# Optimization experiments

Measured on AMD Instinct MI355X. Metric: run time of the kernel, lower is better.

Reference implementation:

```python
import jax, jax.numpy as jnp
import numpy as np
import math

B, L, S, T = 16, 256, 128, 128
Q_DIM, F_DIM, H_DIM, OUT_DIM = 512, 512, 512, 512


def setup_inputs() -> dict:
    key = jax.random.key(0)
    ks = jax.random.split(key, 10)
    inp = {
        "query": jax.random.normal(ks[0], (B, L, Q_DIM), dtype=jnp.float32),
        "src": jax.random.normal(ks[1], (B, S, F_DIM), dtype=jnp.float32),
        "trg": jax.random.normal(ks[2], (B, T, F_DIM), dtype=jnp.float32),
        # LinearAct params (Linear + identity act; out layer uses tanh)
        "Wq": jax.random.normal(ks[3], (Q_DIM, H_DIM), dtype=jnp.float32) / math.sqrt(Q_DIM),
        "bq": jnp.zeros((H_DIM,), dtype=jnp.float32),
        "Ws": jax.random.normal(ks[4], (F_DIM, H_DIM), dtype=jnp.float32) / math.sqrt(F_DIM),
        "bs": jnp.zeros((H_DIM,), dtype=jnp.float32),
        "Wt": jax.random.normal(ks[5], (F_DIM, H_DIM), dtype=jnp.float32) / math.sqrt(F_DIM),
        "bt": jnp.zeros((H_DIM,), dtype=jnp.float32),
        "Wo": jax.random.normal(ks[6], (2 * H_DIM + Q_DIM, OUT_DIM), dtype=jnp.float32) / math.sqrt(2 * H_DIM + Q_DIM),
        "bo": jnp.zeros((OUT_DIM,), dtype=jnp.float32),
    }
    return inp


def reference(query, src, trg, Wq, bq, Ws, bs, Wt, bt, Wo, bo):
    b, l, _ = query.shape
    _, s, f = src.shape
    _, t, _ = trg.shape
    hid_dim = Wq.shape[1]

    q = query @ Wq + bq                              # b, l, h
    # pad one all-zero feature row onto src and trg (as in torch.cat with pad_tensor)
    pad = jnp.zeros((b, 1, f), dtype=src.dtype)
    src_p = jnp.concatenate([src, pad], axis=1)       # b, s+1, f
    trg_p = jnp.concatenate([trg, pad], axis=1)       # b, t+1, f
    s_key = src_p @ Ws + bs                           # b, s+1, h
    t_key = trg_p @ Wt + bt                           # b, t+1, h

    # trilinear scores: b, l, s+1, t+1
    weight = jnp.einsum('blk,bsk,btk->blst', q, s_key, t_key) / math.sqrt(hid_dim)
    # joint softmax over the flattened (s+1)*(t+1) axis
    weight = jax.nn.softmax(weight.reshape(b, l, -1), axis=-1).reshape(b, l, s + 1, t + 1)

    s_ctx = jnp.einsum('blst,bsk->blk', weight, s_key)  # b, l, h
    t_ctx = jnp.einsum('blst,btk->blk', weight, t_key)  # b, l, h

    x = jnp.concatenate([query, s_ctx, t_ctx], axis=-1)  # b, l, q+2h
    return jnp.tanh(x @ Wo + bo)
```

## Files before the change

kernel.cpp:

```cpp
#include <hip/hip_runtime.h>
#include <math.h>

#define HD 512
#define SP 129
#define RPAD 144
#define WPAD 160
#define NBATCH 16
#define MQ 4096
#define SCALE 0.04419417382415922f

typedef _Float16 f16;
typedef _Float16 f16x8 __attribute__((ext_vector_type(8)));
typedef _Float16 f16x4 __attribute__((ext_vector_type(4)));
typedef float f32x4  __attribute__((ext_vector_type(4)));

__device__ __forceinline__ void gload_lds16(const f16* g, f16* l) {
  __builtin_amdgcn_global_load_lds(
      (const __attribute__((address_space(1))) void*)g,
      (__attribute__((address_space(3))) void*)l, 16, 0, 0);
}

__global__ __launch_bounds__(256) void conv_f32_f16(
    const float* __restrict__ a, f16* __restrict__ o, int n)
{
  int base = (blockIdx.x * 256 + threadIdx.x) * 8;
  if (base < n) {
    float4 x = *(const float4*)(a + base);
    float4 y = *(const float4*)(a + base + 4);
    f16x8 v = { (f16)x.x, (f16)x.y, (f16)x.z, (f16)x.w,
                (f16)y.x, (f16)y.y, (f16)y.z, (f16)y.w };
    *(f16x8*)(o + base) = v;
  }
}

__global__ __launch_bounds__(256) void convT_f32_f16(
    const float* __restrict__ W, f16* __restrict__ WT, int K, int N)
{
  __shared__ float t[64][65];
  const int k0 = blockIdx.x * 64, n0 = blockIdx.y * 64;
  const int tid = threadIdx.x;
  const int r = tid >> 4, c4 = (tid & 15) * 4;
  #pragma unroll
  for (int i = 0; i < 4; ++i) {
    int k = r + 16*i;
    float4 v = *(const float4*)(W + (size_t)(k0 + k)*N + n0 + c4);
    t[k][c4] = v.x; t[k][c4+1] = v.y; t[k][c4+2] = v.z; t[k][c4+3] = v.w;
  }
  __syncthreads();
  #pragma unroll
  for (int i = 0; i < 4; ++i) {
    int n = r + 16*i;
    f16x4 v = { (f16)t[c4][n], (f16)t[c4+1][n], (f16)t[c4+2][n], (f16)t[c4+3][n] };
    *(f16x4*)(WT + (size_t)(n0 + n)*K + k0 + c4) = v;
  }
}

template<int NSEG, int MODE>
__global__ __launch_bounds__(256) void gemm_f16(
    const f16* __restrict__ A0, const f16* __restrict__ A1,
    const f16* __restrict__ A2, const f16* __restrict__ WT,
    const float* __restrict__ bias, void* __restrict__ Cv,
    f16* __restrict__ CT, int M, int N)
{
  __shared__ __align__(16) f16 As[64*64];
  __shared__ __align__(16) f16 Bs[64*64];
  const int KTOT = NSEG * 512;
  const int tid  = threadIdx.x;
  const int lane = tid & 63;
  const int w    = tid >> 6;
  const int wr   = w & 1, wc = w >> 1;
  const int fq   = lane >> 4, fr = lane & 15;
  const int bm = blockIdx.x * 64, bn = blockIdx.y * 64;

  f32x4 acc[2][2] = {};

  for (int k0 = 0; k0 < KTOT; k0 += 64) {
    const int seg  = k0 >> 9;
    const f16* Ap  = (NSEG == 1) ? A0 : (seg == 0 ? A0 : (seg == 1 ? A1 : A2));
    const int kloc = k0 & 511;
    #pragma unroll
    for (int i = 0; i < 2; ++i) {
      int idx = tid + 256*i;
      int r = idx >> 3, c = idx & 7;
      const uint4 va = *(const uint4*)(Ap + (size_t)(bm + r)*512 + kloc + c*8);
      const uint4 vb = *(const uint4*)(WT + (size_t)(bn + r)*KTOT + k0 + c*8);
      int o = ((r << 7) + (c << 4)) ^ ((r & 7) << 4);
      *(uint4*)((char*)As + o) = va;
      *(uint4*)((char*)Bs + o) = vb;
    }
    __syncthreads();
    #pragma unroll
    for (int ks = 0; ks < 2; ++ks) {
      f16x8 af[2], bf_[2];
      #pragma unroll
      for (int i = 0; i < 2; ++i) {
        int ra = wr*32 + i*16 + fr;
        int oa = ((ra << 7) + (ks << 6) + (fq << 4)) ^ ((ra & 7) << 4);
        af[i] = *(const f16x8*)((const char*)As + oa);
        int rb = wc*32 + i*16 + fr;
        int ob = ((rb << 7) + (ks << 6) + (fq << 4)) ^ ((rb & 7) << 4);
        bf_[i] = *(const f16x8*)((const char*)Bs + ob);
      }
      #pragma unroll
      for (int i = 0; i < 2; ++i)
        #pragma unroll
        for (int j = 0; j < 2; ++j)
          acc[i][j] = __builtin_amdgcn_mfma_f32_16x16x32_f16(af[i], bf_[j], acc[i][j], 0, 0, 0);
    }
    __syncthreads();
  }

  #pragma unroll
  for (int i = 0; i < 2; ++i) {
    #pragma unroll
    for (int j = 0; j < 2; ++j) {
      int n = bn + wc*32 + j*16 + fr;
      float bv = bias[n];
      if (MODE == 3) {
        const int m0 = bm + wr*32 + i*16 + fq*4;
        f16 vals[4];
        #pragma unroll
        for (int r = 0; r < 4; ++r) {
          int m = m0 + r;
          f16 x = (f16)(acc[i][j][r] + bv);
          vals[r] = x;
          int mo = (m >> 7) * RPAD + (m & 127);
          ((f16*)Cv)[(size_t)mo*N + n] = x;
        }
        f16x4 v4 = { vals[0], vals[1], vals[2], vals[3] };
        *(f16x4*)(CT + ((size_t)(m0 >> 7)*512 + n)*WPAD + (m0 & 127)) = v4;
      } else {
        #pragma unroll
        for (int r = 0; r < 4; ++r) {
          int m = bm + wr*32 + i*16 + fq*4 + r;
          float x = acc[i][j][r] + bv;
          if (MODE == 0) {
            ((f16*)Cv)[(size_t)m*N + n] = (f16)x;
          } else {
            x = fminf(fmaxf(x, -20.f), 20.f);
            float e = __expf(2.0f * x);
            ((float*)Cv)[(size_t)m*N + n] = (e - 1.0f) / (e + 1.0f);
          }
        }
      }
    }
  }
}

__global__ void write_pad_f16(f16* __restrict__ skey, const float* __restrict__ bs,
                              f16* __restrict__ tkey, const float* __restrict__ bt,
                              f16* __restrict__ skeyT, f16* __restrict__ tkeyT)
{
  int i = blockIdx.x * 256 + threadIdx.x;
  int b = i >> 9, n = i & 511;
  for (int r = 128; r < RPAD; ++r) {
    skey[((size_t)b*RPAD + r)*HD + n] = (r == 128) ? (f16)bs[n] : (f16)0.f;
    tkey[((size_t)b*RPAD + r)*HD + n] = (r == 128) ? (f16)bt[n] : (f16)0.f;
  }
  size_t o = ((size_t)b*512 + n)*WPAD;
  for (int c = 128; c < WPAD; ++c) {
    skeyT[o + c] = (c == 128) ? (f16)bs[n] : (f16)0.f;
    tkeyT[o + c] = (c == 128) ? (f16)bt[n] : (f16)0.f;
  }
}

__global__ __launch_bounds__(256) void border_kernel(
    const f16* __restrict__ q_h, const f16* __restrict__ skey,
    const f16* __restrict__ tkey, float* __restrict__ Sb)
{
  const int blk = blockIdx.x;
  const int b = blk >> 3, z = (blk >> 2) & 1, mt = blk & 3;
  const f16* keys = (z ? skey : tkey) + (size_t)b*RPAD*HD;
  const f16* u    = (z ? tkey : skey) + ((size_t)b*RPAD + 128)*HD;
  const int gid0 = b*256 + mt*64;

  __shared__ __align__(16) f16 Ks[RPAD*32];
  const int tid = threadIdx.x, lane = tid & 63, w = tid >> 6;
  const int fq = lane >> 4, fr = lane & 15;

  f32x4 acc[9] = {};

  for (int kt = 0; kt < 16; ++kt) {
    uint4 t0, t1, t2;
    {
      int r0 = tid >> 2, c0 = tid & 3;
      t0 = *(const uint4*)(keys + (size_t)r0*HD + kt*32 + c0*8);
      int r1 = (tid + 256) >> 2, c1 = tid & 3;
      t1 = *(const uint4*)(keys + (size_t)r1*HD + kt*32 + c1*8);
      if (tid < 64) {
        int r2 = (tid + 512) >> 2, c2 = tid & 3;
        t2 = *(const uint4*)(keys + (size_t)r2*HD + kt*32 + c2*8);
      }
    }
    __syncthreads();
    {
      int r0 = tid >> 2, c0 = tid & 3;
      *(uint4*)(&Ks[r0*32 + c0*8]) = t0;
      int r1 = (tid + 256) >> 2;
      *(uint4*)(&Ks[r1*32 + c0*8]) = t1;
      if (tid < 64) {
        int r2 = (tid + 512) >> 2;
        *(uint4*)(&Ks[r2*32 + c0*8]) = t2;
      }
    }
    __syncthreads();
    const f16x8 qf = *(const f16x8*)(q_h + (size_t)(gid0 + w*16 + fr)*HD + kt*32 + fq*8);
    const f16x8 uv = *(const f16x8*)(u + kt*32 + fq*8);
    const f16x8 a = qf * uv;
    #pragma unroll
    for (int j = 0; j < 9; ++j) {
      const f16x8 bfr = *(const f16x8*)(&Ks[(j*16 + fr)*32 + fq*8]);
      acc[j] = __builtin_amdgcn_mfma_f32_16x16x32_f16(a, bfr, acc[j], 0, 0, 0);
    }
  }

  float* dst = Sb + (size_t)z*MQ*RPAD;
  #pragma unroll
  for (int j = 0; j < 9; ++j)
    #pragma unroll
    for (int r = 0; r < 4; ++r)
      dst[(size_t)(gid0 + w*16 + fq*4 + r)*RPAD + j*16 + fr] = acc[j][r];
}

__global__ __launch_bounds__(256, 4) void attn_core(
    const f16* __restrict__ qg,
    const f16* __restrict__ skey,
    const f16* __restrict__ tkey,
    const float* __restrict__ Sb,
    f16* __restrict__ wsn,
    f16* __restrict__ wtn)
{
  __shared__ __align__(16) f16 KB[2*2*128*32];
  __shared__ __align__(16) f16 qs[HD];
  __shared__ float wsA[2][128];
  __shared__ float wtA[2][128];
  __shared__ float redA[4], redB[4], redC[4], redD[4], redE[4];
  __shared__ float cornerP;

  const int tid  = threadIdx.x;
  const int lane = tid & 63;
  const int w    = tid >> 6;
  const int rb   = w & 1;
  const int cb   = w >> 1;
  const int fq   = lane >> 4;
  const int fr   = lane & 15;

  const int gid = ((int)blockIdx.x & 7) * 512 + ((int)blockIdx.x >> 3);
  const int b   = gid >> 8;
  const f16* skg = skey + (size_t)b * RPAD * HD;
  const f16* tkg = tkey + (size_t)b * RPAD * HD;

  if (tid < 64) *(uint4*)(qs + tid*8) = *(const uint4*)(qg + (size_t)gid*HD + tid*8);

  auto stage = [&](int kt, int buf) {
    #pragma unroll
    for (int n = 0; n < 4; ++n) {
      int idx = w*4 + n;
      int key = idx >> 3;
      int rg  = idx & 7;
      const f16* g = (key ? tkg : skg)
                   + (size_t)(rg*16 + (lane >> 2))*HD + kt*32 + (lane & 3)*8;
      f16* l = &KB[((buf*2 + key)*128 + rg*16)*32];
      gload_lds16(g, l);
    }
  };

  f32x4 acc[4][4] = {};

  auto mfma_kt = [&](int kt, int cur) {
    const f16x8 qv = *(const f16x8*)(&qs[kt*32 + fq*8]);
    const int abase = (cur*2 + 0)*128*32;
    const int bbase = (cur*2 + 1)*128*32;
    f16x8 B[4];
    #pragma unroll
    for (int j = 0; j < 4; ++j) {
      int rt = cb*64 + j*16 + fr;
      B[j] = *(const f16x8*)(&KB[bbase + rt*32 + fq*8]);
    }
    __builtin_amdgcn_s_setprio(1);
    #pragma unroll
    for (int i = 0; i < 4; ++i) {
      int rs = rb*64 + i*16 + fr;
      const f16x8 raw = *(const f16x8*)(&KB[abase + rs*32 + fq*8]);
      const f16x8 a = raw * qv;
      #pragma unroll
      for (int j = 0; j < 4; ++j)
        acc[i][j] = __builtin_amdgcn_mfma_f32_16x16x32_f16(a, B[j], acc[i][j], 0, 0, 0);
    }
    __builtin_amdgcn_s_setprio(0);
  };

  stage(0, 0);
  __syncthreads();

  for (int kt = 0; kt < 16; ++kt) {
    const int cur = kt & 1;
    if (kt < 15) {
      stage(kt + 1, cur ^ 1);
      asm volatile("s_waitcnt vmcnt(4)" ::: "memory");
    } else {
      asm volatile("s_waitcnt vmcnt(0)" ::: "memory");
    }
    __builtin_amdgcn_s_barrier();
    mfma_kt(kt, cur);
    __builtin_amdgcn_s_barrier();
  }

  float m = -3e38f;
  #pragma unroll
  for (int i = 0; i < 4; ++i)
    #pragma unroll
    for (int j = 0; j < 4; ++j)
      #pragma unroll
      for (int r = 0; r < 4; ++r) m = fmaxf(m, acc[i][j][r]);
  #pragma unroll
  for (int off = 32; off > 0; off >>= 1) m = fmaxf(m, __shfl_xor(m, off));
  if (lane == 0) redA[w] = m;

  const float* SbT = Sb + (size_t)gid*RPAD;
  const float* SbS = Sb + (size_t)MQ*RPAD + (size_t)gid*RPAD;
  const float btv = (tid < 129) ? SbT[tid] : -3e38f;
  const float bsv = (tid < 128) ? SbS[tid] : -3e38f;
  float bm = fmaxf(btv, bsv);
  #pragma unroll
  for (int off = 32; off > 0; off >>= 1) bm = fmaxf(bm, __shfl_xor(bm, off));
  if (lane == 0) redB[w] = bm;
  __syncthreads();
  const float mraw = fmaxf(
      fmaxf(fmaxf(redA[0], redA[1]), fmaxf(redA[2], redA[3])),
      fmaxf(fmaxf(redB[0], redB[1]), fmaxf(redB[2], redB[3])));

  float csum = 0.f;
  #pragma unroll
  for (int i = 0; i < 4; ++i)
    #pragma unroll
    for (int j = 0; j < 4; ++j)
      #pragma unroll
      for (int r = 0; r < 4; ++r) {
        float p = __expf((acc[i][j][r] - mraw) * SCALE);
        acc[i][j][r] = p;
        csum += p;
      }
  #pragma unroll
  for (int off = 32; off > 0; off >>= 1) csum += __shfl_xor(csum, off);
  if (lane == 0) redC[w] = csum;

  #pragma unroll
  for (int i = 0; i < 4; ++i) {
    #pragma unroll
    for (int r = 0; r < 4; ++r) {
      float rs = acc[i][0][r] + acc[i][1][r] + acc[i][2][r] + acc[i][3][r];
      rs += __shfl_xor(rs, 1); rs += __shfl_xor(rs, 2);
      rs += __shfl_xor(rs, 4); rs += __shfl_xor(rs, 8);
      if (fr == 0) wsA[cb][rb*64 + i*16 + fq*4 + r] = rs;
    }
  }
  #pragma unroll
  for (int j = 0; j < 4; ++j) {
    float cs = 0.f;
    #pragma unroll
    for (int i = 0; i < 4; ++i)
      #pragma unroll
      for (int r = 0; r < 4; ++r) cs += acc[i][j][r];
    cs += __shfl_xor(cs, 16); cs += __shfl_xor(cs, 32);
    if (fq == 0) wtA[rb][cb*64 + j*16 + fr] = cs;
  }

  const float pbt = (tid < 129) ? __expf((btv - mraw) * SCALE) : 0.f;
  const float pbs = (tid < 128) ? __expf((bsv - mraw) * SCALE) : 0.f;
  float sbt = pbt, sbs = pbs;
  #pragma unroll
  for (int off = 32; off > 0; off >>= 1) {
    sbt += __shfl_xor(sbt, off);
    sbs += __shfl_xor(sbs, off);
  }
  if (lane == 0) { redD[w] = sbt; redE[w] = sbs; }
  if (tid == 128) cornerP = pbt;
  __syncthreads();

  const float pbt_sum = redD[0] + redD[1] + redD[2] + redD[3];
  const float pbs_sum = redE[0] + redE[1] + redE[2] + redE[3];
  const float core_sum = redC[0] + redC[1] + redC[2] + redC[3];
  const float invZ = 1.0f / (core_sum + pbt_sum + pbs_sum);

  if (tid < WPAD) {
    float wsv = (tid < 128) ? (wsA[0][tid] + wsA[1][tid] + pbs)
              : (tid == 128) ? pbt_sum : 0.f;
    float wtv = (tid < 128) ? (wtA[0][tid] + wtA[1][tid] + pbt)
              : (tid == 128) ? (pbs_sum + cornerP) : 0.f;
    wsn[(size_t)gid*WPAD + tid] = (f16)(wsv * invZ);
    wtn[(size_t)gid*WPAD + tid] = (f16)(wtv * invZ);
  }
}

__global__ __launch_bounds__(256) void ctx_gemm(
    const f16* __restrict__ wsn, const f16* __restrict__ wtn,
    const f16* __restrict__ skeyT, const f16* __restrict__ tkeyT,
    f16* __restrict__ sctx, f16* __restrict__ tctx)
{
  __shared__ __align__(16) f16 As[64*168];
  __shared__ __align__(16) f16 Bs[64*168];
  const int z = blockIdx.x & 1, b = blockIdx.x >> 1;
  const int mt = blockIdx.y, nt = blockIdx.z;
  const int tid = threadIdx.x, lane = tid & 63, w = tid >> 6;
  const int wr = w & 1, wc = w >> 1;
  const int fq = lane >> 4, fr = lane & 15;

  const f16* A  = (z ? wtn : wsn) + ((size_t)b*256 + mt*64)*WPAD;
  const f16* Bt = (z ? tkeyT : skeyT) + ((size_t)b*512 + nt*64)*WPAD;

  for (int t = tid; t < 1280; t += 256) {
    int r = t / 20, c = t % 20;
    *(uint4*)(&As[r*168 + c*8]) = *(const uint4*)(A + (size_t)r*WPAD + c*8);
    *(uint4*)(&Bs[r*168 + c*8]) = *(const uint4*)(Bt + (size_t)r*WPAD + c*8);
  }
  __syncthreads();

  f32x4 acc[2][2] = {};
  #pragma unroll
  for (int ks = 0; ks < 5; ++ks) {
    f16x8 af[2], bf_[2];
    #pragma unroll
    for (int i = 0; i < 2; ++i) {
      af[i]  = *(const f16x8*)(&As[(wr*32 + i*16 + fr)*168 + ks*32 + fq*8]);
      bf_[i] = *(const f16x8*)(&Bs[(wc*32 + i*16 + fr)*168 + ks*32 + fq*8]);
    }
    #pragma unroll
    for (int i = 0; i < 2; ++i)
      #pragma unroll
      for (int j = 0; j < 2; ++j)
        acc[i][j] = __builtin_amdgcn_mfma_f32_16x16x32_f16(af[i], bf_[j], acc[i][j], 0, 0, 0);
  }

  f16* out = z ? tctx : sctx;
  #pragma unroll
  for (int i = 0; i < 2; ++i)
    #pragma unroll
    for (int j = 0; j < 2; ++j) {
      int col = nt*64 + wc*32 + j*16 + fr;
      #pragma unroll
      for (int r = 0; r < 4; ++r) {
        int row = b*256 + mt*64 + wr*32 + i*16 + fq*4 + r;
        out[(size_t)row*HD + col] = (f16)acc[i][j][r];
      }
    }
}

extern "C" void kernel_launch(void* const* d_in, const int* in_sizes, int n_in,
                              void* d_out, int out_size, void* d_ws, size_t ws_size,
                              hipStream_t stream) {
  (void)in_sizes; (void)n_in; (void)out_size; (void)ws_size;
  const float* query = (const float*)d_in[0];
  const float* src   = (const float*)d_in[1];
  const float* trg   = (const float*)d_in[2];
  const float* Wq    = (const float*)d_in[3];
  const float* bq    = (const float*)d_in[4];
  const float* Wsm   = (const float*)d_in[5];
  const float* bs    = (const float*)d_in[6];
  const float* Wtm   = (const float*)d_in[7];
  const float* bt    = (const float*)d_in[8];
  const float* Wo    = (const float*)d_in[9];
  const float* bo    = (const float*)d_in[10];
  float* out = (float*)d_out;

  char* p = (char*)d_ws;
  f16* query_h = (f16*)p;                 p += (size_t)MQ*HD*2;
  f16* src_h   = (f16*)p;                 p += (size_t)2048*HD*2;
  f16* trg_h   = (f16*)p;                 p += (size_t)2048*HD*2;
  f16* WqT     = (f16*)p;                 p += (size_t)HD*HD*2;
  f16* WsT     = (f16*)p;                 p += (size_t)HD*HD*2;
  f16* WtT     = (f16*)p;                 p += (size_t)HD*HD*2;
  f16* WoT     = (f16*)p;                 p += (size_t)1536*HD*2;
  f16* q_h     = (f16*)p;                 p += (size_t)MQ*HD*2;
  f16* skey    = (f16*)p;                 p += (size_t)NBATCH*RPAD*HD*2;
  f16* tkey    = (f16*)p;                 p += (size_t)NBATCH*RPAD*HD*2;
  f16* skeyT   = (f16*)p;                 p += (size_t)NBATCH*HD*WPAD*2;
  f16* tkeyT   = (f16*)p;                 p += (size_t)NBATCH*HD*WPAD*2;
  f16* wsn     = (f16*)p;                 p += (size_t)MQ*WPAD*2;
  f16* wtn     = (f16*)p;                 p += (size_t)MQ*WPAD*2;
  f16* sctx    = (f16*)p;                 p += (size_t)MQ*HD*2;
  f16* tctx    = (f16*)p;                 p += (size_t)MQ*HD*2;
  float* Sb    = (float*)src_h;

  dim3 blk(256);
  conv_f32_f16<<<dim3(MQ*HD/8/256), blk, 0, stream>>>(query, query_h, MQ*HD);
  conv_f32_f16<<<dim3(2048*HD/8/256), blk, 0, stream>>>(src, src_h, 2048*HD);
  conv_f32_f16<<<dim3(2048*HD/8/256), blk, 0, stream>>>(trg, trg_h, 2048*HD);
  convT_f32_f16<<<dim3(8, 8), blk, 0, stream>>>(Wq, WqT, HD, HD);
  convT_f32_f16<<<dim3(8, 8), blk, 0, stream>>>(Wsm, WsT, HD, HD);
  convT_f32_f16<<<dim3(8, 8), blk, 0, stream>>>(Wtm, WtT, HD, HD);
  convT_f32_f16<<<dim3(24, 8), blk, 0, stream>>>(Wo, WoT, 1536, HD);

  gemm_f16<1,0><<<dim3(64, 8), blk, 0, stream>>>(query_h, nullptr, nullptr, WqT, bq, q_h, nullptr, MQ, HD);
  gemm_f16<1,3><<<dim3(32, 8), blk, 0, stream>>>(src_h, nullptr, nullptr, WsT, bs, skey, skeyT, 2048, HD);
  gemm_f16<1,3><<<dim3(32, 8), blk, 0, stream>>>(trg_h, nullptr, nullptr, WtT, bt, tkey, tkeyT, 2048, HD);
  write_pad_f16<<<dim3(32), blk, 0, stream>>>(skey, bs, tkey, bt, skeyT, tkeyT);

  border_kernel<<<dim3(128), blk, 0, stream>>>(q_h, skey, tkey, Sb);
  attn_core<<<dim3(MQ), blk, 0, stream>>>(q_h, skey, tkey, Sb, wsn, wtn);
  ctx_gemm<<<dim3(32, 4, 8), blk, 0, stream>>>(wsn, wtn, skeyT, tkeyT, sctx, tctx);

  gemm_f16<3,2><<<dim3(64, 8), blk, 0, stream>>>(query_h, sctx, tctx, WoT, bo, out, nullptr, MQ, HD);
}
```

Baseline: 199.7 us.

## Fuse f32→f16 conversion into GEMMs, merge prep launches, swizzle LDS, use exp2

Removes the separate activation-conversion kernels by converting fp32 query/src/trg to f16 inside the GEMM tile loads. Weight transposes and pad writes are merged into one prep kernel, and the three input projections into one launch, which cuts launch count. LDS layouts in border_kernel and attn_core get XOR swizzles to reduce bank conflicts, and exp is replaced by exp2f with prescaled constants. The trade-off is that fp32 activations are now read directly in the GEMMs, and query is re-read and re-converted in the output GEMM.

```diff
diff --git a/kernel.cpp b/kernel.cpp
--- a/kernel.cpp
+++ b/kernel.cpp
@@ -8,6 +8,8 @@
 #define NBATCH 16
 #define MQ 4096
 #define SCALE 0.04419417382415922f
+#define SCLG2E 0.06375871645788f
+#define TANH2E 2.8853900817779268f
 
 typedef _Float16 f16;
 typedef _Float16 f16x8 __attribute__((ext_vector_type(8)));
@@ -20,30 +22,44 @@
       (__attribute__((address_space(3))) void*)l, 16, 0, 0);
 }
 
-__global__ __launch_bounds__(256) void conv_f32_f16(
-    const float* __restrict__ a, f16* __restrict__ o, int n)
+__global__ __launch_bounds__(256) void prep_kernel(
+    const float* __restrict__ Wq, const float* __restrict__ Ws,
+    const float* __restrict__ Wt, const float* __restrict__ Wo,
+    const float* __restrict__ bs, const float* __restrict__ bt,
+    f16* __restrict__ WqT, f16* __restrict__ WsT,
+    f16* __restrict__ WtT, f16* __restrict__ WoT,
+    f16* __restrict__ skey, f16* __restrict__ tkey,
+    f16* __restrict__ skeyT, f16* __restrict__ tkeyT)
 {
-  int base = (blockIdx.x * 256 + threadIdx.x) * 8;
-  if (base < n) {
-    float4 x = *(const float4*)(a + base);
-    float4 y = *(const float4*)(a + base + 4);
-    f16x8 v = { (f16)x.x, (f16)x.y, (f16)x.z, (f16)x.w,
-                (f16)y.x, (f16)y.y, (f16)y.z, (f16)y.w };
-    *(f16x8*)(o + base) = v;
-  }
-}
-
-__global__ __launch_bounds__(256) void convT_f32_f16(
-    const float* __restrict__ W, f16* __restrict__ WT, int K, int N)
-{
+  const int id = blockIdx.x;
+  const int tid = threadIdx.x;
+  if (id >= 384) {
+    int i = (id - 384) * 256 + tid;
+    int b = i >> 9, n = i & 511;
+    for (int r = 128; r < RPAD; ++r) {
+      skey[((size_t)b*RPAD + r)*HD + n] = (r == 128) ? (f16)bs[n] : (f16)0.f;
+      tkey[((size_t)b*RPAD + r)*HD + n] = (r == 128) ? (f16)bt[n] : (f16)0.f;
+    }
+    size_t o = ((size_t)b*512 + n)*WPAD;
+    for (int c = 128; c < WPAD; ++c) {
+      skeyT[o + c] = (c == 128) ? (f16)bs[n] : (f16)0.f;
+      tkeyT[o + c] = (c == 128) ? (f16)bt[n] : (f16)0.f;
+    }
+    return;
+  }
+  const float* W; f16* WT; int K; int rest;
+  if (id < 64)       { W = Wq; WT = WqT; K = 512;  rest = id; }
+  else if (id < 128) { W = Ws; WT = WsT; K = 512;  rest = id - 64; }
+  else if (id < 192) { W = Wt; WT = WtT; K = 512;  rest = id - 128; }
+  else               { W = Wo; WT = WoT; K = 1536; rest = id - 192; }
+  const int k0 = (rest >> 3) * 64, n0 = (rest & 7) * 64;
+
   __shared__ float t[64][65];
-  const int k0 = blockIdx.x * 64, n0 = blockIdx.y * 64;
-  const int tid = threadIdx.x;
   const int r = tid >> 4, c4 = (tid & 15) * 4;
   #pragma unroll
   for (int i = 0; i < 4; ++i) {
     int k = r + 16*i;
-    float4 v = *(const float4*)(W + (size_t)(k0 + k)*N + n0 + c4);
+    float4 v = *(const float4*)(W + (size_t)(k0 + k)*512 + n0 + c4);
     t[k][c4] = v.x; t[k][c4+1] = v.y; t[k][c4+2] = v.z; t[k][c4+3] = v.w;
   }
   __syncthreads();
@@ -55,37 +71,46 @@
   }
 }
 
-template<int NSEG, int MODE>
-__global__ __launch_bounds__(256) void gemm_f16(
-    const f16* __restrict__ A0, const f16* __restrict__ A1,
-    const f16* __restrict__ A2, const f16* __restrict__ WT,
-    const float* __restrict__ bias, void* __restrict__ Cv,
-    f16* __restrict__ CT, int M, int N)
+__global__ __launch_bounds__(256) void gemm_in(
+    const float* __restrict__ query, const float* __restrict__ src,
+    const float* __restrict__ trg,
+    const f16* __restrict__ WqT, const f16* __restrict__ WsT,
+    const f16* __restrict__ WtT,
+    const float* __restrict__ bq, const float* __restrict__ bsv,
+    const float* __restrict__ btv,
+    f16* __restrict__ q_h, f16* __restrict__ skey, f16* __restrict__ tkey,
+    f16* __restrict__ skeyT, f16* __restrict__ tkeyT)
 {
   __shared__ __align__(16) f16 As[64*64];
   __shared__ __align__(16) f16 Bs[64*64];
-  const int KTOT = NSEG * 512;
+  const int x = blockIdx.x;
+  const float* A; const f16* WT; const float* bias; int bm; int iskey;
+  f16 *Ch, *CT;
+  if (x < 64)      { A = query; WT = WqT; bias = bq;  bm = x*64;      iskey = 0; Ch = q_h;  CT = nullptr; }
+  else if (x < 96) { A = src;   WT = WsT; bias = bsv; bm = (x-64)*64; iskey = 1; Ch = skey; CT = skeyT; }
+  else             { A = trg;   WT = WtT; bias = btv; bm = (x-96)*64; iskey = 1; Ch = tkey; CT = tkeyT; }
+  const int bn = blockIdx.y * 64;
   const int tid  = threadIdx.x;
   const int lane = tid & 63;
   const int w    = tid >> 6;
   const int wr   = w & 1, wc = w >> 1;
   const int fq   = lane >> 4, fr = lane & 15;
-  const int bm = blockIdx.x * 64, bn = blockIdx.y * 64;
 
   f32x4 acc[2][2] = {};
 
-  for (int k0 = 0; k0 < KTOT; k0 += 64) {
-    const int seg  = k0 >> 9;
-    const f16* Ap  = (NSEG == 1) ? A0 : (seg == 0 ? A0 : (seg == 1 ? A1 : A2));
-    const int kloc = k0 & 511;
+  for (int k0 = 0; k0 < 512; k0 += 64) {
     #pragma unroll
     for (int i = 0; i < 2; ++i) {
       int idx = tid + 256*i;
       int r = idx >> 3, c = idx & 7;
-      const uint4 va = *(const uint4*)(Ap + (size_t)(bm + r)*512 + kloc + c*8);
-      const uint4 vb = *(const uint4*)(WT + (size_t)(bn + r)*KTOT + k0 + c*8);
+      const float* ap = A + (size_t)(bm + r)*512 + k0 + c*8;
+      float4 x0 = *(const float4*)ap;
+      float4 x1 = *(const float4*)(ap + 4);
+      f16x8 va = { (f16)x0.x, (f16)x0.y, (f16)x0.z, (f16)x0.w,
+                   (f16)x1.x, (f16)x1.y, (f16)x1.z, (f16)x1.w };
+      const uint4 vb = *(const uint4*)(WT + (size_t)(bn + r)*512 + k0 + c*8);
       int o = ((r << 7) + (c << 4)) ^ ((r & 7) << 4);
-      *(uint4*)((char*)As + o) = va;
+      *(f16x8*)((char*)As + o) = va;
       *(uint4*)((char*)Bs + o) = vb;
     }
     __syncthreads();
@@ -116,16 +141,16 @@
     for (int j = 0; j < 2; ++j) {
       int n = bn + wc*32 + j*16 + fr;
       float bv = bias[n];
-      if (MODE == 3) {
+      if (iskey) {
         const int m0 = bm + wr*32 + i*16 + fq*4;
         f16 vals[4];
         #pragma unroll
         for (int r = 0; r < 4; ++r) {
           int m = m0 + r;
-          f16 x = (f16)(acc[i][j][r] + bv);
-          vals[r] = x;
+          f16 xx = (f16)(acc[i][j][r] + bv);
+          vals[r] = xx;
           int mo = (m >> 7) * RPAD + (m & 127);
-          ((f16*)Cv)[(size_t)mo*N + n] = x;
+          Ch[(size_t)mo*512 + n] = xx;
         }
         f16x4 v4 = { vals[0], vals[1], vals[2], vals[3] };
         *(f16x4*)(CT + ((size_t)(m0 >> 7)*512 + n)*WPAD + (m0 & 127)) = v4;
@@ -133,34 +158,10 @@
         #pragma unroll
         for (int r = 0; r < 4; ++r) {
           int m = bm + wr*32 + i*16 + fq*4 + r;
-          float x = acc[i][j][r] + bv;
-          if (MODE == 0) {
-            ((f16*)Cv)[(size_t)m*N + n] = (f16)x;
-          } else {
-            x = fminf(fmaxf(x, -20.f), 20.f);
-            float e = __expf(2.0f * x);
-            ((float*)Cv)[(size_t)m*N + n] = (e - 1.0f) / (e + 1.0f);
-          }
+          Ch[(size_t)m*512 + n] = (f16)(acc[i][j][r] + bv);
         }
       }
     }
-  }
-}
-
-__global__ void write_pad_f16(f16* __restrict__ skey, const float* __restrict__ bs,
-                              f16* __restrict__ tkey, const float* __restrict__ bt,
-                              f16* __restrict__ skeyT, f16* __restrict__ tkeyT)
-{
-  int i = blockIdx.x * 256 + threadIdx.x;
-  int b = i >> 9, n = i & 511;
-  for (int r = 128; r < RPAD; ++r) {
-    skey[((size_t)b*RPAD + r)*HD + n] = (r == 128) ? (f16)bs[n] : (f16)0.f;
-    tkey[((size_t)b*RPAD + r)*HD + n] = (r == 128) ? (f16)bt[n] : (f16)0.f;
-  }
-  size_t o = ((size_t)b*512 + n)*WPAD;
-  for (int c = 128; c < WPAD; ++c) {
-    skeyT[o + c] = (c == 128) ? (f16)bs[n] : (f16)0.f;
-    tkeyT[o + c] = (c == 128) ? (f16)bt[n] : (f16)0.f;
   }
 }
 
@@ -177,6 +178,8 @@
   __shared__ __align__(16) f16 Ks[RPAD*32];
   const int tid = threadIdx.x, lane = tid & 63, w = tid >> 6;
   const int fq = lane >> 4, fr = lane & 15;
+  const int wslot = ((tid & 3) ^ ((tid >> 3) & 3)) * 8;
+  const int rslot = ((fq ^ ((fr >> 1) & 3))) * 8;
 
   f32x4 acc[9] = {};
 
@@ -185,22 +188,22 @@
     {
       int r0 = tid >> 2, c0 = tid & 3;
       t0 = *(const uint4*)(keys + (size_t)r0*HD + kt*32 + c0*8);
-      int r1 = (tid + 256) >> 2, c1 = tid & 3;
-      t1 = *(const uint4*)(keys + (size_t)r1*HD + kt*32 + c1*8);
+      int r1 = (tid + 256) >> 2;
+      t1 = *(const uint4*)(keys + (size_t)r1*HD + kt*32 + c0*8);
       if (tid < 64) {
-        int r2 = (tid + 512) >> 2, c2 = tid & 3;
-        t2 = *(const uint4*)(keys + (size_t)r2*HD + kt*32 + c2*8);
+        int r2 = (tid + 512) >> 2;
+        t2 = *(const uint4*)(keys + (size_t)r2*HD + kt*32 + c0*8);
       }
     }
     __syncthreads();
     {
-      int r0 = tid >> 2, c0 = tid & 3;
-      *(uint4*)(&Ks[r0*32 + c0*8]) = t0;
+      int r0 = tid >> 2;
+      *(uint4*)(&Ks[r0*32 + wslot]) = t0;
       int r1 = (tid + 256) >> 2;
-      *(uint4*)(&Ks[r1*32 + c0*8]) = t1;
+      *(uint4*)(&Ks[r1*32 + wslot]) = t1;
       if (tid < 64) {
         int r2 = (tid + 512) >> 2;
-        *(uint4*)(&Ks[r2*32 + c0*8]) = t2;
+        *(uint4*)(&Ks[r2*32 + wslot]) = t2;
       }
     }
     __syncthreads();
@@ -209,7 +212,7 @@
     const f16x8 a = qf * uv;
     #pragma unroll
     for (int j = 0; j < 9; ++j) {
-      const f16x8 bfr = *(const f16x8*)(&Ks[(j*16 + fr)*32 + fq*8]);
+      const f16x8 bfr = *(const f16x8*)(&Ks[(j*16 + fr)*32 + rslot]);
       acc[j] = __builtin_amdgcn_mfma_f32_16x16x32_f16(a, bfr, acc[j], 0, 0, 0);
     }
   }
@@ -244,6 +247,8 @@
   const int cb   = w >> 1;
   const int fq   = lane >> 4;
   const int fr   = lane & 15;
+  const int so   = (fq ^ ((fr >> 1) & 3)) << 3;
+  const int gc   = ((lane & 3) ^ ((lane >> 3) & 3)) * 8;
 
   const int gid = ((int)blockIdx.x & 7) * 512 + ((int)blockIdx.x >> 3);
   const int b   = gid >> 8;
@@ -259,7 +264,7 @@
       int key = idx >> 3;
       int rg  = idx & 7;
       const f16* g = (key ? tkg : skg)
-                   + (size_t)(rg*16 + (lane >> 2))*HD + kt*32 + (lane & 3)*8;
+                   + (size_t)(rg*16 + (lane >> 2))*HD + kt*32 + gc;
       f16* l = &KB[((buf*2 + key)*128 + rg*16)*32];
       gload_lds16(g, l);
     }
@@ -275,13 +280,13 @@
     #pragma unroll
     for (int j = 0; j < 4; ++j) {
       int rt = cb*64 + j*16 + fr;
-      B[j] = *(const f16x8*)(&KB[bbase + rt*32 + fq*8]);
+      B[j] = *(const f16x8*)(&KB[bbase + rt*32 + so]);
     }
     __builtin_amdgcn_s_setprio(1);
     #pragma unroll
     for (int i = 0; i < 4; ++i) {
       int rs = rb*64 + i*16 + fr;
-      const f16x8 raw = *(const f16x8*)(&KB[abase + rs*32 + fq*8]);
+      const f16x8 raw = *(const f16x8*)(&KB[abase + rs*32 + so]);
       const f16x8 a = raw * qv;
       #pragma unroll
       for (int j = 0; j < 4; ++j)
@@ -337,7 +342,7 @@
     for (int j = 0; j < 4; ++j)
       #pragma unroll
       for (int r = 0; r < 4; ++r) {
-        float p = __expf((acc[i][j][r] - mraw) * SCALE);
+        float p = exp2f((acc[i][j][r] - mraw) * SCLG2E);
         acc[i][j][r] = p;
         csum += p;
       }
@@ -366,8 +371,8 @@
     if (fq == 0) wtA[rb][cb*64 + j*16 + fr] = cs;
   }
 
-  const float pbt = (tid < 129) ? __expf((btv - mraw) * SCALE) : 0.f;
-  const float pbs = (tid < 128) ? __expf((bsv - mraw) * SCALE) : 0.f;
+  const float pbt = (tid < 129) ? exp2f((btv - mraw) * SCLG2E) : 0.f;
+  const float pbs = (tid < 128) ? exp2f((bsv - mraw) * SCLG2E) : 0.f;
   float sbt = pbt, sbs = pbs;
   #pragma unroll
   for (int off = 32; off > 0; off >>= 1) {
@@ -442,6 +447,82 @@
       for (int r = 0; r < 4; ++r) {
         int row = b*256 + mt*64 + wr*32 + i*16 + fq*4 + r;
         out[(size_t)row*HD + col] = (f16)acc[i][j][r];
+      }
+    }
+}
+
+__global__ __launch_bounds__(256) void gemm_out(
+    const float* __restrict__ query, const f16* __restrict__ sctx,
+    const f16* __restrict__ tctx, const f16* __restrict__ WoT,
+    const float* __restrict__ bias, float* __restrict__ C)
+{
+  __shared__ __align__(16) f16 As[64*64];
+  __shared__ __align__(16) f16 Bs[64*64];
+  const int tid  = threadIdx.x;
+  const int lane = tid & 63;
+  const int w    = tid >> 6;
+  const int wr   = w & 1, wc = w >> 1;
+  const int fq   = lane >> 4, fr = lane & 15;
+  const int bm = blockIdx.x * 64, bn = blockIdx.y * 64;
+
+  f32x4 acc[2][2] = {};
+
+  for (int k0 = 0; k0 < 1536; k0 += 64) {
+    const int seg  = k0 >> 9;
+    const int kloc = k0 & 511;
+    #pragma unroll
+    for (int i = 0; i < 2; ++i) {
+      int idx = tid + 256*i;
+      int r = idx >> 3, c = idx & 7;
+      int o = ((r << 7) + (c << 4)) ^ ((r & 7) << 4);
+      if (seg == 0) {
+        const float* ap = query + (size_t)(bm + r)*512 + kloc + c*8;
+        float4 x0 = *(const float4*)ap;
+        float4 x1 = *(const float4*)(ap + 4);
+        f16x8 va = { (f16)x0.x, (f16)x0.y, (f16)x0.z, (f16)x0.w,
+                     (f16)x1.x, (f16)x1.y, (f16)x1.z, (f16)x1.w };
+        *(f16x8*)((char*)As + o) = va;
+      } else {
+        const f16* Ap = (seg == 1) ? sctx : tctx;
+        *(uint4*)((char*)As + o) = *(const uint4*)(Ap + (size_t)(bm + r)*512 + kloc + c*8);
+      }
+      *(uint4*)((char*)Bs + o) = *(const uint4*)(WoT + (size_t)(bn + r)*1536 + k0 + c*8);
+    }
+    __syncthreads();
+    #pragma unroll
+    for (int ks = 0; ks < 2; ++ks) {
+      f16x8 af[2], bf_[2];
+      #pragma unroll
+      for (int i = 0; i < 2; ++i) {
+        int ra = wr*32 + i*16 + fr;
+        int oa = ((ra << 7) + (ks << 6) + (fq << 4)) ^ ((ra & 7) << 4);
+        af[i] = *(const f16x8*)((const char*)As + oa);
+        int rb = wc*32 + i*16 + fr;
+        int ob = ((rb << 7) + (ks << 6) + (fq << 4)) ^ ((rb & 7) << 4);
+        bf_[i] = *(const f16x8*)((const char*)Bs + ob);
+      }
+      #pragma unroll
+      for (int i = 0; i < 2; ++i)
+        #pragma unroll
+        for (int j = 0; j < 2; ++j)
+          acc[i][j] = __builtin_amdgcn_mfma_f32_16x16x32_f16(af[i], bf_[j], acc[i][j], 0, 0, 0);
+    }
+    __syncthreads();
+  }
+
+  #pragma unroll
+  for (int i = 0; i < 2; ++i)
+    #pragma unroll
+    for (int j = 0; j < 2; ++j) {
+      int n = bn + wc*32 + j*16 + fr;
+      float bv = bias[n];
+      #pragma unroll
+      for (int r = 0; r < 4; ++r) {
+        int m = bm + wr*32 + i*16 + fq*4 + r;
+        float xx = acc[i][j][r] + bv;
+        xx = fminf(fmaxf(xx, -20.f), 20.f);
+        float e = exp2f(TANH2E * xx);
+        C[(size_t)m*HD + n] = (e - 1.0f) / (e + 1.0f);
       }
     }
 }
@@ -464,41 +545,30 @@
   float* out = (float*)d_out;
 
   char* p = (char*)d_ws;
-  f16* query_h = (f16*)p;                 p += (size_t)MQ*HD*2;
-  f16* src_h   = (f16*)p;                 p += (size_t)2048*HD*2;
-  f16* trg_h   = (f16*)p;                 p += (size_t)2048*HD*2;
-  f16* WqT     = (f16*)p;                 p += (size_t)HD*HD*2;
-  f16* WsT     = (f16*)p;                 p += (size_t)HD*HD*2;
-  f16* WtT     = (f16*)p;                 p += (size_t)HD*HD*2;
-  f16* WoT     = (f16*)p;                 p += (size_t)1536*HD*2;
-  f16* q_h     = (f16*)p;                 p += (size_t)MQ*HD*2;
-  f16* skey    = (f16*)p;                 p += (size_t)NBATCH*RPAD*HD*2;
-  f16* tkey    = (f16*)p;                 p += (size_t)NBATCH*RPAD*HD*2;
-  f16* skeyT   = (f16*)p;                 p += (size_t)NBATCH*HD*WPAD*2;
-  f16* tkeyT   = (f16*)p;                 p += (size_t)NBATCH*HD*WPAD*2;
-  f16* wsn     = (f16*)p;                 p += (size_t)MQ*WPAD*2;
-  f16* wtn     = (f16*)p;                 p += (size_t)MQ*WPAD*2;
-  f16* sctx    = (f16*)p;                 p += (size_t)MQ*HD*2;
-  f16* tctx    = (f16*)p;                 p += (size_t)MQ*HD*2;
-  float* Sb    = (float*)src_h;
+  f16* WqT   = (f16*)p;  p += (size_t)HD*HD*2;
+  f16* WsT   = (f16*)p;  p += (size_t)HD*HD*2;
+  f16* WtT   = (f16*)p;  p += (size_t)HD*HD*2;
+  f16* WoT   = (f16*)p;  p += (size_t)1536*HD*2;
+  f16* q_h   = (f16*)p;  p += (size_t)MQ*HD*2;
+  f16* skey  = (f16*)p;  p += (size_t)NBATCH*RPAD*HD*2;
+  f16* tkey  = (f16*)p;  p += (size_t)NBATCH*RPAD*HD*2;
+  f16* skeyT = (f16*)p;  p += (size_t)NBATCH*HD*WPAD*2;
+  f16* tkeyT = (f16*)p;  p += (size_t)NBATCH*HD*WPAD*2;
+  f16* wsn   = (f16*)p;  p += (size_t)MQ*WPAD*2;
+  f16* wtn   = (f16*)p;  p += (size_t)MQ*WPAD*2;
+  f16* sctx  = (f16*)p;  p += (size_t)MQ*HD*2;
+  f16* tctx  = (f16*)p;  p += (size_t)MQ*HD*2;
+  float* Sb  = (float*)p; p += (size_t)2*MQ*RPAD*4;
 
   dim3 blk(256);
-  conv_f32_f16<<<dim3(MQ*HD/8/256), blk, 0, stream>>>(query, query_h, MQ*HD);
-  conv_f32_f16<<<dim3(2048*HD/8/256), blk, 0, stream>>>(src, src_h, 2048*HD);
-  conv_f32_f16<<<dim3(2048*HD/8/256), blk, 0, stream>>>(trg, trg_h, 2048*HD);
-  convT_f32_f16<<<dim3(8, 8), blk, 0, stream>>>(Wq, WqT, HD, HD);
-  convT_f32_f16<<<dim3(8, 8), blk, 0, stream>>>(Wsm, WsT, HD, HD);
-  convT_f32_f16<<<dim3(8, 8), blk, 0, stream>>>(Wtm, WtT, HD, HD);
-  convT_f32_f16<<<dim3(24, 8), blk, 0, stream>>>(Wo, WoT, 1536, HD);
-
-  gemm_f16<1,0><<<dim3(64, 8), blk, 0, stream>>>(query_h, nullptr, nullptr, WqT, bq, q_h, nullptr, MQ, HD);
-  gemm_f16<1,3><<<dim3(32, 8), blk, 0, stream>>>(src_h, nullptr, nullptr, WsT, bs, skey, skeyT, 2048, HD);
-  gemm_f16<1,3><<<dim3(32, 8), blk, 0, stream>>>(trg_h, nullptr, nullptr, WtT, bt, tkey, tkeyT, 2048, HD);
-  write_pad_f16<<<dim3(32), blk, 0, stream>>>(skey, bs, tkey, bt, skeyT, tkeyT);
-
+  prep_kernel<<<dim3(416), blk, 0, stream>>>(Wq, Wsm, Wtm, Wo, bs, bt,
+                                             WqT, WsT, WtT, WoT,
+                                             skey, tkey, skeyT, tkeyT);
+  gemm_in<<<dim3(128, 8), blk, 0, stream>>>(query, src, trg, WqT, WsT, WtT,
+                                            bq, bs, bt, q_h, skey, tkey,
+                                            skeyT, tkeyT);
   border_kernel<<<dim3(128), blk, 0, stream>>>(q_h, skey, tkey, Sb);
   attn_core<<<dim3(MQ), blk, 0, stream>>>(q_h, skey, tkey, Sb, wsn, wtn);
   ctx_gemm<<<dim3(32, 4, 8), blk, 0, stream>>>(wsn, wtn, skeyT, tkeyT, sctx, tctx);
-
-  gemm_f16<3,2><<<dim3(64, 8), blk, 0, stream>>>(query_h, sctx, tctx, WoT, bo, out, nullptr, MQ, HD);
-}
+  gemm_out<<<dim3(64, 8), blk, 0, stream>>>(query, sctx, tctx, WoT, bo, out);
+}
```

Result: faster. 192.9 us (-3.4%).
